# Kernel optimization log

Hardware: AMD Instinct MI355X
Metric: run time of the kernel (lower is better)

Reference implementation:

```python
import jax, jax.numpy as jnp
import numpy as np

D_MODEL = 256      # num_nodes == d_model (forced by pre_relation mask shape)
MW = 2             # moving_window (hardcoded '2' in MPNN reshape)
STRIDE = 1
DECAY = 0.7
INPUT_DIM = 64
OUTPUT_DIM = 64
BN_EPS = 1e-5


def _mask_matrix():
    # Mask_Matrix: block (i,j) of size d_model x d_model equals decay**|i-j|
    blocks = DECAY ** np.abs(np.arange(MW)[:, None] - np.arange(MW)[None, :])
    return jnp.asarray(np.kron(blocks, np.ones((D_MODEL, D_MODEL))).astype(np.float32))


def _bn(h, w, b):
    # training-mode BatchNorm1d over channel-last layout [B, N, C]
    mu = h.mean(axis=(0, 1))
    var = h.var(axis=(0, 1))  # biased variance, as torch uses for normalization
    return (h - mu) * jax.lax.rsqrt(var + BN_EPS) * w + b


def setup_inputs() -> dict:
    key = jax.random.key(0)
    ks = jax.random.split(key, 4)
    bs, scale_num = 16, 17
    x = jax.random.normal(ks[0], (bs, scale_num, D_MODEL, INPUT_DIM), jnp.float32)
    # mapping2 weights scaled small to keep the dot-product softmax well conditioned
    w_map2 = jax.random.normal(ks[1], (INPUT_DIM, INPUT_DIM), jnp.float32) * 0.05
    b_map2 = jnp.zeros((INPUT_DIM,), jnp.float32)
    bn0_w = jnp.ones((INPUT_DIM,), jnp.float32)
    bn0_b = jnp.zeros((INPUT_DIM,), jnp.float32)
    th0_w = jax.random.normal(ks[2], (OUTPUT_DIM, INPUT_DIM), jnp.float32) / np.float32(np.sqrt(INPUT_DIM))
    th0_b = jnp.zeros((OUTPUT_DIM,), jnp.float32)
    th1_w = jax.random.normal(ks[3], (OUTPUT_DIM, INPUT_DIM), jnp.float32) / np.float32(np.sqrt(INPUT_DIM))
    th1_b = jnp.zeros((OUTPUT_DIM,), jnp.float32)
    bn1_w = jnp.ones((OUTPUT_DIM,), jnp.float32)
    bn1_b = jnp.zeros((OUTPUT_DIM,), jnp.float32)
    return dict(x=x, w_map2=w_map2, b_map2=b_map2, bn0_w=bn0_w, bn0_b=bn0_b,
                th0_w=th0_w, th0_b=th0_b, th1_w=th1_w, th1_b=th1_b,
                bn1_w=bn1_w, bn1_b=bn1_b)


def reference(x, w_map2, b_map2, bn0_w, bn0_b, th0_w, th0_b, th1_w, th1_b, bn1_w, bn1_b):
    bs, S, N, F = x.shape
    L = (S - MW) // STRIDE + 1  # num_windows from F.unfold
    # WindowConv_Graph + transpose(2,3) + reshape: X[b,l,m,n,f] = x[b, l*stride+m, n, f]
    idx = np.arange(L)[:, None] * STRIDE + np.arange(MW)[None, :]
    X = x[:, idx].reshape(bs * L, MW * N, F)  # [B', N1, F]

    # Dot_Graph_Construction_weights (N1 != d_model -> mapping2 branch)
    nf = X @ w_map2.T + b_map2                       # [B', N1, F]
    adj = jnp.einsum('bnf,bmf->bnm', nf, nf)         # [B', N1, N1]
    eye = jnp.eye(MW * N, dtype=x.dtype)
    adj = jax.nn.leaky_relu(adj - eye * 1e8)
    adj = jax.nn.softmax(adj, axis=-1) + eye

    # decay mask multiply
    adj = adj * _mask_matrix()

    # BatchNorm over input_dim channels
    xb = _bn(nf, bn0_w, bn0_b)

    # MPNN_mk_v2, field=2, way='sum'
    out = (adj @ xb) @ th0_w.T + th0_b               # hop 1
    adj2 = adj @ adj
    out = out + (adj2 @ xb) @ th1_w.T + th1_b        # hop 2
    out = jax.nn.leaky_relu(_bn(out, bn1_w, bn1_b))

    # pooling over the moving_window axis (mean), then over windows (mean)
    out = out.reshape(bs, L, MW, N, OUTPUT_DIM).mean(axis=2)
    return out.mean(axis=1)  # [bs, num_nodes, output_dim]
```

## Files before the change

kernel.cpp:

```cpp
#include <hip/hip_runtime.h>


typedef unsigned short u16;
typedef __bf16 bf16x8 __attribute__((ext_vector_type(8)));
typedef float f32x4 __attribute__((ext_vector_type(4)));
typedef unsigned int u32x4 __attribute__((ext_vector_type(4)));

#define MFMA16(a, b, c) __builtin_amdgcn_mfma_f32_16x16x32_bf16(a, b, c, 0, 0, 0)

#define BSZ 16
#define SNUM 17
#define FD 64
#define NB 256
#define N1 512
#define SL_ELEMS 16384
#define Y_ELEMS (BSZ * SNUM * SL_ELEMS)

#define WM_O 0
#define BM_O 4096
#define B0W_O 4160
#define B0B_O 4224
#define T0W_O 4288
#define T0B_O 8384
#define T1W_O 8448
#define T1B_O 12544
#define B1W_O 12608
#define B1B_O 12672
#define P_TOT 12736

#define SLAB2_O 32768
#define RED_O 65536
#define SCR_O 65792
#define LDS_U16 (SCR_O + 16 * 640)

__device__ __forceinline__ float bf2f(u16 u) {
    union { unsigned int i; float f; } v;
    v.i = ((unsigned int)u) << 16;
    return v.f;
}
__device__ __forceinline__ u16 f2bu(float f) {
    __bf16 h = (__bf16)f;
    return __builtin_bit_cast(u16, h);
}
__device__ __forceinline__ u16 f2bf(float f) {
    unsigned int u = __builtin_bit_cast(unsigned int, f);
    unsigned int r = (u + 0x7fffu + ((u >> 16) & 1u)) >> 16;
    return (u16)r;
}
__device__ __forceinline__ bf16x8 ld8g(const u16* p) {
    return __builtin_bit_cast(bf16x8, *reinterpret_cast<const u32x4*>(p));
}

__global__ __launch_bounds__(256) void k_prep(
    const void* p0, const void* p1, const void* p2, const void* p3,
    const void* p4, const void* p5, const void* p6, const void* p7,
    const void* p8, const void* p9, int* __restrict__ flagOut,
    u16* __restrict__ pc, float* __restrict__ stats) {
    const int tid = threadIdx.x, lane = tid & 63;
    int z = 0, bc = 0;
    const unsigned int* w = (const unsigned int*)p0;
    for (int i = lane; i < 2048; i += 64) {
        const unsigned int v = w[i];
        z += ((v & 0xffffu) == 0u);
        bc += (v >> 14) & 1;
    }
#pragma unroll
    for (int o = 1; o < 64; o <<= 1) {
        z += __shfl_xor(z, o);
        bc += __shfl_xor(bc, o);
    }
    const int flag = (z > 1024 || bc > 256) ? 1 : 0;
    if (blockIdx.x == 0) {
        if (tid == 0) *flagOut = flag;
        if (tid < 256) stats[tid] = 0.f;
    }
    const int i = blockIdx.x * 256 + tid;
    if (i >= P_TOT) return;
    const void* src;
    int si;
    if (i < BM_O)        { src = p0; si = i; }
    else if (i < B0W_O)  { src = p1; si = i - BM_O; }
    else if (i < B0B_O)  { src = p2; si = i - B0W_O; }
    else if (i < T0W_O)  { src = p3; si = i - B0B_O; }
    else if (i < T0B_O)  { src = p4; si = i - T0W_O; }
    else if (i < T1W_O)  { src = p5; si = i - T0B_O; }
    else if (i < T1B_O)  { src = p6; si = i - T1W_O; }
    else if (i < B1W_O)  { src = p7; si = i - T1B_O; }
    else if (i < B1B_O)  { src = p8; si = i - B1W_O; }
    else                 { src = p9; si = i - B1B_O; }
    pc[i] = flag ? f2bf(((const float*)src)[si]) : ((const u16*)src)[si];
}

__global__ __launch_bounds__(256) void k_y(const void* __restrict__ xv,
                                           const int* __restrict__ flag,
                                           const u16* __restrict__ pc,
                                           u16* __restrict__ y,
                                           float* __restrict__ gstats) {
    const int slice = blockIdx.x;
    const int tid = threadIdx.x, wave = tid >> 6, lane = tid & 63;
    const int quad = lane >> 4, l16 = lane & 15;
    __shared__ float red[128];
    if (tid < 128) red[tid] = 0.f;
    const int isf32 = *flag;

    f32x4 acc[4][4];
#pragma unroll
    for (int i = 0; i < 4; i++)
#pragma unroll
        for (int j = 0; j < 4; j++) acc[i][j] = (f32x4){0.f, 0.f, 0.f, 0.f};

    bf16x8 bfr[4][2];
#pragma unroll
    for (int nt = 0; nt < 4; nt++)
#pragma unroll
        for (int kh = 0; kh < 2; kh++)
            bfr[nt][kh] = ld8g(pc + WM_O + (nt * 16 + l16) * 64 + kh * 32 + quad * 8);

    const float* xf = (const float*)xv + (size_t)slice * SL_ELEMS;
    const u16* xh = (const u16*)xv + (size_t)slice * SL_ELEMS;

#pragma unroll
    for (int mt = 0; mt < 4; mt++) {
        const int row = wave * 64 + mt * 16 + l16;
        bf16x8 a0, a1;
        if (isf32) {
            const float* r0 = xf + row * 64 + quad * 8;
            f32x4 v0 = *(const f32x4*)r0;
            f32x4 v1 = *(const f32x4*)(r0 + 4);
            f32x4 v2 = *(const f32x4*)(r0 + 32);
            f32x4 v3 = *(const f32x4*)(r0 + 36);
#pragma unroll
            for (int j = 0; j < 4; j++) {
                a0[j] = (__bf16)v0[j]; a0[4 + j] = (__bf16)v1[j];
                a1[j] = (__bf16)v2[j]; a1[4 + j] = (__bf16)v3[j];
            }
        } else {
            a0 = ld8g(xh + row * 64 + quad * 8);
            a1 = ld8g(xh + row * 64 + 32 + quad * 8);
        }
#pragma unroll
        for (int nt = 0; nt < 4; nt++)
            acc[mt][nt] = MFMA16(a1, bfr[nt][1], MFMA16(a0, bfr[nt][0], acc[mt][nt]));
    }

    u16* ys = y + (size_t)slice * SL_ELEMS;
    float s1[4] = {0.f, 0.f, 0.f, 0.f}, s2[4] = {0.f, 0.f, 0.f, 0.f};
#pragma unroll
    for (int nt = 0; nt < 4; nt++) {
        const int col = nt * 16 + l16;
        const float bias = bf2f(pc[BM_O + col]);
#pragma unroll
        for (int mt = 0; mt < 4; mt++)
#pragma unroll
            for (int r = 0; r < 4; r++) {
                const int row = wave * 64 + mt * 16 + quad * 4 + r;
                const float v = acc[mt][nt][r] + bias;
                ys[row * 64 + col] = f2bu(v);
                s1[nt] += v;
                s2[nt] += v * v;
            }
        s1[nt] += __shfl_xor(s1[nt], 16); s1[nt] += __shfl_xor(s1[nt], 32);
        s2[nt] += __shfl_xor(s2[nt], 16); s2[nt] += __shfl_xor(s2[nt], 32);
    }
    __syncthreads();
    if (quad == 0) {
#pragma unroll
        for (int nt = 0; nt < 4; nt++) {
            atomicAdd(&red[nt * 16 + l16], s1[nt]);
            atomicAdd(&red[64 + nt * 16 + l16], s2[nt]);
        }
    }
    __syncthreads();
    const int s = slice % SNUM;
    const float wgt = (s == 0 || s == SNUM - 1) ? 1.f : 2.f;
    if (tid < 128) atomicAdd(&gstats[tid], red[tid] * wgt);
}

__global__ __launch_bounds__(1024)
__attribute__((amdgpu_waves_per_eu(4, 4)))
void k_mega(
    const u16* __restrict__ y, float* __restrict__ stats,
    const u16* __restrict__ pc, u16* __restrict__ opre) {
    __shared__ u16 lds[LDS_U16];
    u16* slab1 = lds;
    u16* slab2 = lds + SLAB2_O;
    float* red = (float*)(lds + RED_O);
    const int tid = threadIdx.x, w = tid >> 6, lane = tid & 63;
    const int quad = lane >> 4, l16 = lane & 15;
    u16* scr = lds + SCR_O + w * 640;
    const int p = blockIdx.x, b = p >> 4, l = p & 15;
    const f32x4 ZERO4 = (f32x4){0.f, 0.f, 0.f, 0.f};

    if (tid < 128) red[tid] = 0.f;

    const float cinv = 1.f / 131072.f;
    const int fme = tid & 63;
    float mu0 = stats[fme] * cinv;
    float vr0 = fmaxf(stats[64 + fme] * cinv - mu0 * mu0, 0.f);
    const float scale_f = rsqrtf(vr0 + 1e-5f) * bf2f(pc[B0W_O + fme]);
    const float shift_f = bf2f(pc[B0B_O + fme]) - mu0 * scale_f;

    const u16* ybase = y + (size_t)(b * SNUM + l) * SL_ELEMS;
#pragma unroll
    for (int i = 0; i < 4; i++) {
        const int gid = i * 1024 + tid, n = gid >> 3, g = gid & 7;
        *(u32x4*)(slab1 + n * 64 + ((g ^ (n & 7)) << 3)) =
            *(const u32x4*)(ybase + n * 64 + g * 8);
    }
    __syncthreads();

#pragma unroll
    for (int i = 0; i < 4; i++) {
        const int gn = (tid >> 6) + i * 16;
        union { u16 u[8]; u32x4 v; } pk;
#pragma unroll
        for (int j = 0; j < 8; j++) {
            const int n = gn * 8 + j;
            const u16 raw = slab1[n * 64 + (((fme >> 3) ^ (n & 7)) << 3) + (fme & 7)];
            pk.u[j] = f2bu(bf2f(raw) * scale_f + shift_f);
        }
        *(u32x4*)(slab2 + fme * 512 + ((gn ^ fme) << 3)) = pk.v;
    }
    __syncthreads();

    bf16x8 a[2][2];
#pragma unroll
    for (int st = 0; st < 2; st++)
#pragma unroll
        for (int h = 0; h < 2; h++) {
            const int row = w * 32 + st * 16 + l16;
            a[st][h] = *(const bf16x8*)(slab1 + row * 64 + (((h * 4 + quad) ^ (row & 7)) << 3));
        }

    const float mb = (w < 8) ? 0.7f : (1.0f / 0.7f);
    const float me = (w < 8) ? (1.0f / 0.7f) : 1.0f;

#pragma unroll 1
    for (int pass = 0; pass < 2; pass++) {
        f32x4 oacc[2][4];
        f32x4 lsum[2];
#pragma unroll
        for (int st = 0; st < 2; st++) {
            lsum[st] = ZERO4;
#pragma unroll
            for (int ft = 0; ft < 4; ft++) oacc[st][ft] = ZERO4;
        }

#pragma unroll 1
        for (int c = 0; c < 8; c++) {
            if (c == 4) {
#pragma unroll
                for (int st = 0; st < 2; st++)
#pragma unroll
                    for (int r = 0; r < 4; r++) lsum[st][r] *= mb;
            }
            const float lmf = ((w >= 8) == (c >= 4)) ? 0.f : -0.5145731728f;
#pragma unroll
            for (int ch = 0; ch < 2; ch++) {
                const int colbase = c * 64 + ch * 32;
                f32x4 S[2][2];
#pragma unroll
                for (int jt = 0; jt < 2; jt++) {
                    const int rj = colbase + jt * 16 + l16;
                    const bf16x8 b0 = *(const bf16x8*)(slab1 + rj * 64 + ((quad ^ (rj & 7)) << 3));
                    const bf16x8 b1 = *(const bf16x8*)(slab1 + rj * 64 + (((4 + quad) ^ (rj & 7)) << 3));
#pragma unroll
                    for (int st = 0; st < 2; st++)
                        S[st][jt] = MFMA16(a[st][1], b1, MFMA16(a[st][0], b0, ZERO4));
                }
                bf16x8 pa[2];
#pragma unroll
                for (int st = 0; st < 2; st++) {
                    const int rowbase = w * 32 + st * 16;
#pragma unroll
                    for (int jt = 0; jt < 2; jt++)
#pragma unroll
                        for (int r = 0; r < 4; r++) {
                            const float s = S[st][jt][r];
                            const float m2 = s > 0.f ? 1.44269504f : 0.0144269504f;
                            float pv = exp2f(fminf(fmaf(s, m2, lmf), 86.f));
                            if (colbase + jt * 16 == rowbase && l16 == quad * 4 + r) pv = 0.f;
                            lsum[st][r] += pv;
                            scr[(quad * 4 + r) * 40 + jt * 16 + l16] = f2bu(pv);
                        }
                    pa[st] = *(const bf16x8*)(scr + l16 * 40 + quad * 8);
                }
#pragma unroll
                for (int ft = 0; ft < 4; ft++) {
                    const int f = ft * 16 + l16, gn = c * 8 + ch * 4 + quad;
                    const bf16x8 bv = *(const bf16x8*)(slab2 + f * 512 + ((gn ^ f) << 3));
                    oacc[0][ft] = MFMA16(pa[0], bv, oacc[0][ft]);
                    oacc[1][ft] = MFMA16(pa[1], bv, oacc[1][ft]);
                }
            }
        }
#pragma unroll
        for (int st = 0; st < 2; st++)
#pragma unroll
            for (int r = 0; r < 4; r++) {
                lsum[st][r] += __shfl_xor(lsum[st][r], 1);
                lsum[st][r] += __shfl_xor(lsum[st][r], 2);
                lsum[st][r] += __shfl_xor(lsum[st][r], 4);
                lsum[st][r] += __shfl_xor(lsum[st][r], 8);
            }

        if (pass == 0) {
#pragma unroll
            for (int st = 0; st < 2; st++) {
                f32x4 inv;
#pragma unroll
                for (int r = 0; r < 4; r++) inv[r] = __builtin_amdgcn_rcpf(lsum[st][r] * me);
#pragma unroll
                for (int ft = 0; ft < 4; ft++)
#pragma unroll
                    for (int r = 0; r < 4; r++) {
                        const int i = w * 32 + st * 16 + quad * 4 + r;
                        const int f = ft * 16 + l16;
                        const float xbv = bf2f(slab2[f * 512 + (((i >> 3) ^ f) << 3) + (i & 7)]);
                        oacc[st][ft][r] = oacc[st][ft][r] * inv[r] + xbv;
                    }
            }
            __syncthreads();
#pragma unroll
            for (int st = 0; st < 2; st++)
#pragma unroll
                for (int ft = 0; ft < 4; ft++)
#pragma unroll
                    for (int r = 0; r < 4; r++) {
                        const int i = w * 32 + st * 16 + quad * 4 + r;
                        const int f = ft * 16 + l16;
                        slab2[f * 512 + (((i >> 3) ^ f) << 3) + (i & 7)] = f2bu(oacc[st][ft][r]);
                    }
            __syncthreads();
        } else {
            float s1a[4] = {0.f, 0.f, 0.f, 0.f}, s2a[4] = {0.f, 0.f, 0.f, 0.f};
#pragma unroll
            for (int st = 0; st < 2; st++) {
                f32x4 inv;
#pragma unroll
                for (int r = 0; r < 4; r++) inv[r] = __builtin_amdgcn_rcpf(lsum[st][r] * me);
#pragma unroll
                for (int ft = 0; ft < 4; ft++)
#pragma unroll
                    for (int r = 0; r < 4; r++) {
                        const int i = w * 32 + st * 16 + quad * 4 + r;
                        const int f = ft * 16 + l16;
                        const float o1 = bf2f(slab2[f * 512 + (((i >> 3) ^ f) << 3) + (i & 7)]);
                        oacc[st][ft][r] = oacc[st][ft][r] * inv[r] + o1;
                    }
                bf16x8 a1[2], a2[2];
                const int irow = w * 32 + st * 16 + l16;
#pragma unroll
                for (int h = 0; h < 2; h++)
#pragma unroll
                    for (int j = 0; j < 8; j++) {
                        const int f = h * 32 + quad * 8 + j;
                        const u16 raw = slab2[f * 512 + (((irow >> 3) ^ f) << 3) + (irow & 7)];
                        a1[h][j] = __builtin_bit_cast(__bf16, raw);
                    }
#pragma unroll
                for (int h = 0; h < 2; h++) {
#pragma unroll
                    for (int ftl = 0; ftl < 2; ftl++)
#pragma unroll
                        for (int r = 0; r < 4; r++)
                            scr[(quad * 4 + r) * 40 + ftl * 16 + l16] = f2bu(oacc[st][2 * h + ftl][r]);
                    a2[h] = *(const bf16x8*)(scr + l16 * 40 + quad * 8);
                }
                f32x4 pacc[4];
#pragma unroll
                for (int ot = 0; ot < 4; ot++) {
                    const int o = ot * 16 + l16;
                    const float bias = bf2f(pc[T0B_O + o]) + bf2f(pc[T1B_O + o]);
                    pacc[ot] = (f32x4){bias, bias, bias, bias};
                }
#pragma unroll
                for (int h = 0; h < 2; h++)
#pragma unroll
                    for (int ot = 0; ot < 4; ot++) {
                        const int o = ot * 16 + l16;
                        bf16x8 w0f = ld8g(pc + T0W_O + o * 64 + h * 32 + quad * 8);
                        bf16x8 w1f = ld8g(pc + T1W_O + o * 64 + h * 32 + quad * 8);
                        pacc[ot] = MFMA16(a1[h], w0f, pacc[ot]);
                        pacc[ot] = MFMA16(a2[h], w1f, pacc[ot]);
                    }
#pragma unroll
                for (int ot = 0; ot < 4; ot++)
#pragma unroll
                    for (int r = 0; r < 4; r++) {
                        const int i = w * 32 + st * 16 + quad * 4 + r;
                        const int o = ot * 16 + l16;
                        const float v = pacc[ot][r];
                        s1a[ot] += v;
                        s2a[ot] += v * v;
                        opre[(size_t)p * (N1 * FD) + (size_t)i * 64 + o] = f2bu(v);
                    }
            }
#pragma unroll
            for (int ot = 0; ot < 4; ot++) {
                s1a[ot] += __shfl_xor(s1a[ot], 16); s1a[ot] += __shfl_xor(s1a[ot], 32);
                s2a[ot] += __shfl_xor(s2a[ot], 16); s2a[ot] += __shfl_xor(s2a[ot], 32);
            }
            if (quad == 0) {
#pragma unroll
                for (int ot = 0; ot < 4; ot++) {
                    atomicAdd(&red[ot * 16 + l16], s1a[ot]);
                    atomicAdd(&red[64 + ot * 16 + l16], s2a[ot]);
                }
            }
            __syncthreads();
            if (tid < 128) atomicAdd(&stats[128 + tid], red[tid]);
        }
    }
}

__global__ __launch_bounds__(256) void k_final(const u16* __restrict__ op,
                                               const float* __restrict__ stats,
                                               const u16* __restrict__ pc,
                                               float* __restrict__ out) {
    const int o = blockIdx.x * 256 + threadIdx.x;
    const int f = o & 63, n = (o >> 6) & 255, b = o >> 14;
    const float inv = 1.f / 131072.f;
    const float mu = stats[128 + f] * inv;
    const float var = fmaxf(stats[192 + f] * inv - mu * mu, 0.f);
    const float rs = rsqrtf(var + 1e-5f);
    const float scale = rs * bf2f(pc[B1W_O + f]);
    const float shift = bf2f(pc[B1B_O + f]) - mu * scale;
    float acc = 0.f;
    for (int l = 0; l < 16; l++) {
        const size_t pb = (size_t)(b * 16 + l) * N1 * FD;
#pragma unroll
        for (int m = 0; m < 2; m++) {
            float v = bf2f(op[pb + (size_t)(m * 256 + n) * 64 + f]);
            v = v * scale + shift;
            acc += (v > 0.f ? v : 0.01f * v);
        }
    }
    out[o] = acc * (1.f / 32.f);
}

extern "C" void kernel_launch(void* const* d_in, const int* in_sizes, int n_in,
                              void* d_out, int out_size, void* d_ws, size_t ws_size,
                              hipStream_t stream) {
    char* ws = (char*)d_ws;
    size_t off = 0;
    auto alloc = [&](size_t bytes) { void* pp = ws + off; off += (bytes + 255) & ~(size_t)255; return pp; };
    u16* y = (u16*)alloc((size_t)Y_ELEMS * 2);
    u16* opre = (u16*)alloc((size_t)NB * N1 * FD * 2);
    u16* pc = (u16*)alloc(P_TOT * 2);
    float* stats = (float*)alloc(256 * 4);
    int* flag = (int*)alloc(256);
    float* out = (float*)d_out;

    k_prep<<<50, 256, 0, stream>>>(d_in[1], d_in[2], d_in[3], d_in[4], d_in[5],
                                   d_in[6], d_in[7], d_in[8], d_in[9], d_in[10],
                                   flag, pc, stats);
    k_y<<<BSZ * SNUM, 256, 0, stream>>>(d_in[0], flag, pc, y, stats);
    k_mega<<<NB, 1024, 0, stream>>>(y, stats, pc, opre);
    k_final<<<1024, 256, 0, stream>>>(opre, stats, pc, out);
}
```

Baseline: 200.8 us.

## Split mega kernel into two hop kernels with row-half blocks

Replaces the single k_mega kernel (256 blocks, each handling all 512 rows over two hop passes) with two kernels launched over 512 blocks, where each block handles one 256-row half. The first hop result is written to a global z1 image and reloaded by the second kernel, which also recomputes the staging of the input slab. The aim is to fill more CUs, since 256 blocks of 1024 threads underuse the device. In exchange it adds an extra launch, a global round trip for the intermediate, and duplicated score and softmax computation across the two kernels.

```diff
diff --git a/kernel.cpp b/kernel.cpp
--- a/kernel.cpp
+++ b/kernel.cpp
@@ -176,11 +176,154 @@
     if (tid < 128) atomicAdd(&gstats[tid], red[tid] * wgt);
 }
 
+__device__ __forceinline__ void stage_slab1(u16* slab1, const u16* ybase,
+                                            int tid) {
+#pragma unroll
+    for (int i = 0; i < 4; i++) {
+        const int gid = i * 1024 + tid, n = gid >> 3, g = gid & 7;
+        *(u32x4*)(slab1 + n * 64 + ((g ^ (n & 7)) << 3)) =
+            *(const u32x4*)(ybase + n * 64 + g * 8);
+    }
+}
+
 __global__ __launch_bounds__(1024)
 __attribute__((amdgpu_waves_per_eu(4, 4)))
-void k_mega(
-    const u16* __restrict__ y, float* __restrict__ stats,
-    const u16* __restrict__ pc, u16* __restrict__ opre) {
+void k_h1(const u16* __restrict__ y, const float* __restrict__ stats,
+          const u16* __restrict__ pc, u16* __restrict__ z1img) {
+    __shared__ u16 lds[LDS_U16];
+    u16* slab1 = lds;
+    u16* slab2 = lds + SLAB2_O;
+    const int tid = threadIdx.x, w = tid >> 6, lane = tid & 63;
+    const int quad = lane >> 4, l16 = lane & 15;
+    u16* scr = lds + SCR_O + w * 640;
+    const int g = blockIdx.x, p = g >> 1, half = g & 1;
+    const int b = p >> 4, l = p & 15;
+    const f32x4 ZERO4 = (f32x4){0.f, 0.f, 0.f, 0.f};
+
+    const float cinv = 1.f / 131072.f;
+    const int fme = tid & 63;
+    float mu0 = stats[fme] * cinv;
+    float vr0 = fmaxf(stats[64 + fme] * cinv - mu0 * mu0, 0.f);
+    const float scale_f = rsqrtf(vr0 + 1e-5f) * bf2f(pc[B0W_O + fme]);
+    const float shift_f = bf2f(pc[B0B_O + fme]) - mu0 * scale_f;
+
+    const u16* ybase = y + (size_t)(b * SNUM + l) * SL_ELEMS;
+    stage_slab1(slab1, ybase, tid);
+    __syncthreads();
+
+#pragma unroll
+    for (int i = 0; i < 4; i++) {
+        const int gn = (tid >> 6) + i * 16;
+        union { u16 u[8]; u32x4 v; } pk;
+#pragma unroll
+        for (int j = 0; j < 8; j++) {
+            const int n = gn * 8 + j;
+            const u16 raw = slab1[n * 64 + (((fme >> 3) ^ (n & 7)) << 3) + (fme & 7)];
+            pk.u[j] = f2bu(bf2f(raw) * scale_f + shift_f);
+        }
+        *(u32x4*)(slab2 + fme * 512 + ((gn ^ fme) << 3)) = pk.v;
+    }
+    __syncthreads();
+
+    const int rowbase = half * 256 + w * 16;
+    bf16x8 a[2];
+#pragma unroll
+    for (int h = 0; h < 2; h++) {
+        const int row = rowbase + l16;
+        a[h] = *(const bf16x8*)(slab1 + row * 64 + (((h * 4 + quad) ^ (row & 7)) << 3));
+    }
+
+    const float mb = (half == 0) ? 0.7f : (1.0f / 0.7f);
+    const float me = (half == 0) ? (1.0f / 0.7f) : 1.0f;
+
+    f32x4 oacc[4];
+    f32x4 lsum = ZERO4;
+#pragma unroll
+    for (int ft = 0; ft < 4; ft++) oacc[ft] = ZERO4;
+
+#pragma unroll 1
+    for (int c = 0; c < 8; c++) {
+        if (c == 4) {
+#pragma unroll
+            for (int r = 0; r < 4; r++) lsum[r] *= mb;
+        }
+        const float lmf = ((half == 1) == (c >= 4)) ? 0.f : -0.5145731728f;
+#pragma unroll
+        for (int ch = 0; ch < 2; ch++) {
+            const int colbase = c * 64 + ch * 32;
+            f32x4 S[2];
+#pragma unroll
+            for (int jt = 0; jt < 2; jt++) {
+                const int rj = colbase + jt * 16 + l16;
+                const bf16x8 b0 = *(const bf16x8*)(slab1 + rj * 64 + ((quad ^ (rj & 7)) << 3));
+                const bf16x8 b1 = *(const bf16x8*)(slab1 + rj * 64 + (((4 + quad) ^ (rj & 7)) << 3));
+                S[jt] = MFMA16(a[1], b1, MFMA16(a[0], b0, ZERO4));
+            }
+#pragma unroll
+            for (int jt = 0; jt < 2; jt++)
+#pragma unroll
+                for (int r = 0; r < 4; r++) {
+                    const float s = S[jt][r];
+                    const float m2 = s > 0.f ? 1.44269504f : 0.0144269504f;
+                    float pv = exp2f(fminf(fmaf(s, m2, lmf), 86.f));
+                    if (colbase + jt * 16 == rowbase && l16 == quad * 4 + r) pv = 0.f;
+                    lsum[r] += pv;
+                    scr[(quad * 4 + r) * 40 + jt * 16 + l16] = f2bu(pv);
+                }
+            const bf16x8 pa = *(const bf16x8*)(scr + l16 * 40 + quad * 8);
+#pragma unroll
+            for (int ft = 0; ft < 4; ft++) {
+                const int f = ft * 16 + l16, gn = c * 8 + ch * 4 + quad;
+                const bf16x8 bv = *(const bf16x8*)(slab2 + f * 512 + ((gn ^ f) << 3));
+                oacc[ft] = MFMA16(pa, bv, oacc[ft]);
+            }
+        }
+    }
+#pragma unroll
+    for (int r = 0; r < 4; r++) {
+        lsum[r] += __shfl_xor(lsum[r], 1);
+        lsum[r] += __shfl_xor(lsum[r], 2);
+        lsum[r] += __shfl_xor(lsum[r], 4);
+        lsum[r] += __shfl_xor(lsum[r], 8);
+    }
+
+    f32x4 inv;
+#pragma unroll
+    for (int r = 0; r < 4; r++) inv[r] = __builtin_amdgcn_rcpf(lsum[r] * me);
+#pragma unroll
+    for (int ft = 0; ft < 4; ft++)
+#pragma unroll
+        for (int r = 0; r < 4; r++) {
+            const int i = rowbase + quad * 4 + r;
+            const int f = ft * 16 + l16;
+            const float xbv = bf2f(slab2[f * 512 + (((i >> 3) ^ f) << 3) + (i & 7)]);
+            oacc[ft][r] = oacc[ft][r] * inv[r] + xbv;
+        }
+    __syncthreads();
+#pragma unroll
+    for (int ft = 0; ft < 4; ft++)
+#pragma unroll
+        for (int r = 0; r < 4; r++) {
+            const int i = rowbase + quad * 4 + r;
+            const int f = ft * 16 + l16;
+            slab2[f * 512 + (((i >> 3) ^ f) << 3) + (i & 7)] = f2bu(oacc[ft][r]);
+        }
+    __syncthreads();
+    {
+        const int fr = tid >> 4, seg = tid & 15;
+        const int off = (((half * 32) ^ (fr & 32)) << 3) + seg * 16;
+        u16* dst = z1img + (size_t)p * 32768 + fr * 512 + off;
+        const u16* srcp = slab2 + fr * 512 + off;
+        *(u32x4*)(dst) = *(const u32x4*)(srcp);
+        *(u32x4*)(dst + 8) = *(const u32x4*)(srcp + 8);
+    }
+}
+
+__global__ __launch_bounds__(1024)
+__attribute__((amdgpu_waves_per_eu(4, 4)))
+void k_h2(const u16* __restrict__ y, const u16* __restrict__ z1img,
+          float* __restrict__ stats, const u16* __restrict__ pc,
+          u16* __restrict__ opre) {
     __shared__ u16 lds[LDS_U16];
     u16* slab1 = lds;
     u16* slab2 = lds + SLAB2_O;
@@ -188,230 +331,159 @@
     const int tid = threadIdx.x, w = tid >> 6, lane = tid & 63;
     const int quad = lane >> 4, l16 = lane & 15;
     u16* scr = lds + SCR_O + w * 640;
-    const int p = blockIdx.x, b = p >> 4, l = p & 15;
+    const int g = blockIdx.x, p = g >> 1, half = g & 1;
+    const int b = p >> 4, l = p & 15;
     const f32x4 ZERO4 = (f32x4){0.f, 0.f, 0.f, 0.f};
 
     if (tid < 128) red[tid] = 0.f;
 
-    const float cinv = 1.f / 131072.f;
-    const int fme = tid & 63;
-    float mu0 = stats[fme] * cinv;
-    float vr0 = fmaxf(stats[64 + fme] * cinv - mu0 * mu0, 0.f);
-    const float scale_f = rsqrtf(vr0 + 1e-5f) * bf2f(pc[B0W_O + fme]);
-    const float shift_f = bf2f(pc[B0B_O + fme]) - mu0 * scale_f;
-
     const u16* ybase = y + (size_t)(b * SNUM + l) * SL_ELEMS;
+    stage_slab1(slab1, ybase, tid);
+
+    const u16* zsrc = z1img + (size_t)p * 32768;
 #pragma unroll
     for (int i = 0; i < 4; i++) {
-        const int gid = i * 1024 + tid, n = gid >> 3, g = gid & 7;
-        *(u32x4*)(slab1 + n * 64 + ((g ^ (n & 7)) << 3)) =
-            *(const u32x4*)(ybase + n * 64 + g * 8);
-    }
-    __syncthreads();
-
-#pragma unroll
-    for (int i = 0; i < 4; i++) {
-        const int gn = (tid >> 6) + i * 16;
-        union { u16 u[8]; u32x4 v; } pk;
+        const int gid = i * 1024 + tid;
+        *(u32x4*)(slab2 + gid * 8) = *(const u32x4*)(zsrc + gid * 8);
+    }
+    __syncthreads();
+
+    const int rowbase = half * 256 + w * 16;
+    bf16x8 a[2];
+#pragma unroll
+    for (int h = 0; h < 2; h++) {
+        const int row = rowbase + l16;
+        a[h] = *(const bf16x8*)(slab1 + row * 64 + (((h * 4 + quad) ^ (row & 7)) << 3));
+    }
+
+    const float mb = (half == 0) ? 0.7f : (1.0f / 0.7f);
+    const float me = (half == 0) ? (1.0f / 0.7f) : 1.0f;
+
+    f32x4 oacc[4];
+    f32x4 lsum = ZERO4;
+#pragma unroll
+    for (int ft = 0; ft < 4; ft++) oacc[ft] = ZERO4;
+
+#pragma unroll 1
+    for (int c = 0; c < 8; c++) {
+        if (c == 4) {
+#pragma unroll
+            for (int r = 0; r < 4; r++) lsum[r] *= mb;
+        }
+        const float lmf = ((half == 1) == (c >= 4)) ? 0.f : -0.5145731728f;
+#pragma unroll
+        for (int ch = 0; ch < 2; ch++) {
+            const int colbase = c * 64 + ch * 32;
+            f32x4 S[2];
+#pragma unroll
+            for (int jt = 0; jt < 2; jt++) {
+                const int rj = colbase + jt * 16 + l16;
+                const bf16x8 b0 = *(const bf16x8*)(slab1 + rj * 64 + ((quad ^ (rj & 7)) << 3));
+                const bf16x8 b1 = *(const bf16x8*)(slab1 + rj * 64 + (((4 + quad) ^ (rj & 7)) << 3));
+                S[jt] = MFMA16(a[1], b1, MFMA16(a[0], b0, ZERO4));
+            }
+#pragma unroll
+            for (int jt = 0; jt < 2; jt++)
+#pragma unroll
+                for (int r = 0; r < 4; r++) {
+                    const float s = S[jt][r];
+                    const float m2 = s > 0.f ? 1.44269504f : 0.0144269504f;
+                    float pv = exp2f(fminf(fmaf(s, m2, lmf), 86.f));
+                    if (colbase + jt * 16 == rowbase && l16 == quad * 4 + r) pv = 0.f;
+                    lsum[r] += pv;
+                    scr[(quad * 4 + r) * 40 + jt * 16 + l16] = f2bu(pv);
+                }
+            const bf16x8 pa = *(const bf16x8*)(scr + l16 * 40 + quad * 8);
+#pragma unroll
+            for (int ft = 0; ft < 4; ft++) {
+                const int f = ft * 16 + l16, gn = c * 8 + ch * 4 + quad;
+                const bf16x8 bv = *(const bf16x8*)(slab2 + f * 512 + ((gn ^ f) << 3));
+                oacc[ft] = MFMA16(pa, bv, oacc[ft]);
+            }
+        }
+    }
+#pragma unroll
+    for (int r = 0; r < 4; r++) {
+        lsum[r] += __shfl_xor(lsum[r], 1);
+        lsum[r] += __shfl_xor(lsum[r], 2);
+        lsum[r] += __shfl_xor(lsum[r], 4);
+        lsum[r] += __shfl_xor(lsum[r], 8);
+    }
+
+    float s1a[4] = {0.f, 0.f, 0.f, 0.f}, s2a[4] = {0.f, 0.f, 0.f, 0.f};
+    f32x4 inv;
+#pragma unroll
+    for (int r = 0; r < 4; r++) inv[r] = __builtin_amdgcn_rcpf(lsum[r] * me);
+#pragma unroll
+    for (int ft = 0; ft < 4; ft++)
+#pragma unroll
+        for (int r = 0; r < 4; r++) {
+            const int i = rowbase + quad * 4 + r;
+            const int f = ft * 16 + l16;
+            const float o1 = bf2f(slab2[f * 512 + (((i >> 3) ^ f) << 3) + (i & 7)]);
+            oacc[ft][r] = oacc[ft][r] * inv[r] + o1;
+        }
+    bf16x8 a1[2], a2[2];
+    const int irow = rowbase + l16;
+#pragma unroll
+    for (int h = 0; h < 2; h++)
 #pragma unroll
         for (int j = 0; j < 8; j++) {
-            const int n = gn * 8 + j;
-            const u16 raw = slab1[n * 64 + (((fme >> 3) ^ (n & 7)) << 3) + (fme & 7)];
-            pk.u[j] = f2bu(bf2f(raw) * scale_f + shift_f);
-        }
-        *(u32x4*)(slab2 + fme * 512 + ((gn ^ fme) << 3)) = pk.v;
-    }
-    __syncthreads();
-
-    bf16x8 a[2][2];
-#pragma unroll
-    for (int st = 0; st < 2; st++)
-#pragma unroll
-        for (int h = 0; h < 2; h++) {
-            const int row = w * 32 + st * 16 + l16;
-            a[st][h] = *(const bf16x8*)(slab1 + row * 64 + (((h * 4 + quad) ^ (row & 7)) << 3));
-        }
-
-    const float mb = (w < 8) ? 0.7f : (1.0f / 0.7f);
-    const float me = (w < 8) ? (1.0f / 0.7f) : 1.0f;
-
-#pragma unroll 1
-    for (int pass = 0; pass < 2; pass++) {
-        f32x4 oacc[2][4];
-        f32x4 lsum[2];
-#pragma unroll
-        for (int st = 0; st < 2; st++) {
-            lsum[st] = ZERO4;
-#pragma unroll
-            for (int ft = 0; ft < 4; ft++) oacc[st][ft] = ZERO4;
-        }
-
-#pragma unroll 1
-        for (int c = 0; c < 8; c++) {
-            if (c == 4) {
-#pragma unroll
-                for (int st = 0; st < 2; st++)
-#pragma unroll
-                    for (int r = 0; r < 4; r++) lsum[st][r] *= mb;
-            }
-            const float lmf = ((w >= 8) == (c >= 4)) ? 0.f : -0.5145731728f;
-#pragma unroll
-            for (int ch = 0; ch < 2; ch++) {
-                const int colbase = c * 64 + ch * 32;
-                f32x4 S[2][2];
-#pragma unroll
-                for (int jt = 0; jt < 2; jt++) {
-                    const int rj = colbase + jt * 16 + l16;
-                    const bf16x8 b0 = *(const bf16x8*)(slab1 + rj * 64 + ((quad ^ (rj & 7)) << 3));
-                    const bf16x8 b1 = *(const bf16x8*)(slab1 + rj * 64 + (((4 + quad) ^ (rj & 7)) << 3));
-#pragma unroll
-                    for (int st = 0; st < 2; st++)
-                        S[st][jt] = MFMA16(a[st][1], b1, MFMA16(a[st][0], b0, ZERO4));
-                }
-                bf16x8 pa[2];
-#pragma unroll
-                for (int st = 0; st < 2; st++) {
-                    const int rowbase = w * 32 + st * 16;
-#pragma unroll
-                    for (int jt = 0; jt < 2; jt++)
-#pragma unroll
-                        for (int r = 0; r < 4; r++) {
-                            const float s = S[st][jt][r];
-                            const float m2 = s > 0.f ? 1.44269504f : 0.0144269504f;
-                            float pv = exp2f(fminf(fmaf(s, m2, lmf), 86.f));
-                            if (colbase + jt * 16 == rowbase && l16 == quad * 4 + r) pv = 0.f;
-                            lsum[st][r] += pv;
-                            scr[(quad * 4 + r) * 40 + jt * 16 + l16] = f2bu(pv);
-                        }
-                    pa[st] = *(const bf16x8*)(scr + l16 * 40 + quad * 8);
-                }
-#pragma unroll
-                for (int ft = 0; ft < 4; ft++) {
-                    const int f = ft * 16 + l16, gn = c * 8 + ch * 4 + quad;
-                    const bf16x8 bv = *(const bf16x8*)(slab2 + f * 512 + ((gn ^ f) << 3));
-                    oacc[0][ft] = MFMA16(pa[0], bv, oacc[0][ft]);
-                    oacc[1][ft] = MFMA16(pa[1], bv, oacc[1][ft]);
-                }
-            }
-        }
-#pragma unroll
-        for (int st = 0; st < 2; st++)
-#pragma unroll
-            for (int r = 0; r < 4; r++) {
-                lsum[st][r] += __shfl_xor(lsum[st][r], 1);
-                lsum[st][r] += __shfl_xor(lsum[st][r], 2);
-                lsum[st][r] += __shfl_xor(lsum[st][r], 4);
-                lsum[st][r] += __shfl_xor(lsum[st][r], 8);
-            }
-
-        if (pass == 0) {
-#pragma unroll
-            for (int st = 0; st < 2; st++) {
-                f32x4 inv;
-#pragma unroll
-                for (int r = 0; r < 4; r++) inv[r] = __builtin_amdgcn_rcpf(lsum[st][r] * me);
-#pragma unroll
-                for (int ft = 0; ft < 4; ft++)
-#pragma unroll
-                    for (int r = 0; r < 4; r++) {
-                        const int i = w * 32 + st * 16 + quad * 4 + r;
-                        const int f = ft * 16 + l16;
-                        const float xbv = bf2f(slab2[f * 512 + (((i >> 3) ^ f) << 3) + (i & 7)]);
-                        oacc[st][ft][r] = oacc[st][ft][r] * inv[r] + xbv;
-                    }
-            }
-            __syncthreads();
-#pragma unroll
-            for (int st = 0; st < 2; st++)
-#pragma unroll
-                for (int ft = 0; ft < 4; ft++)
-#pragma unroll
-                    for (int r = 0; r < 4; r++) {
-                        const int i = w * 32 + st * 16 + quad * 4 + r;
-                        const int f = ft * 16 + l16;
-                        slab2[f * 512 + (((i >> 3) ^ f) << 3) + (i & 7)] = f2bu(oacc[st][ft][r]);
-                    }
-            __syncthreads();
-        } else {
-            float s1a[4] = {0.f, 0.f, 0.f, 0.f}, s2a[4] = {0.f, 0.f, 0.f, 0.f};
-#pragma unroll
-            for (int st = 0; st < 2; st++) {
-                f32x4 inv;
-#pragma unroll
-                for (int r = 0; r < 4; r++) inv[r] = __builtin_amdgcn_rcpf(lsum[st][r] * me);
-#pragma unroll
-                for (int ft = 0; ft < 4; ft++)
-#pragma unroll
-                    for (int r = 0; r < 4; r++) {
-                        const int i = w * 32 + st * 16 + quad * 4 + r;
-                        const int f = ft * 16 + l16;
-                        const float o1 = bf2f(slab2[f * 512 + (((i >> 3) ^ f) << 3) + (i & 7)]);
-                        oacc[st][ft][r] = oacc[st][ft][r] * inv[r] + o1;
-                    }
-                bf16x8 a1[2], a2[2];
-                const int irow = w * 32 + st * 16 + l16;
-#pragma unroll
-                for (int h = 0; h < 2; h++)
-#pragma unroll
-                    for (int j = 0; j < 8; j++) {
-                        const int f = h * 32 + quad * 8 + j;
-                        const u16 raw = slab2[f * 512 + (((irow >> 3) ^ f) << 3) + (irow & 7)];
-                        a1[h][j] = __builtin_bit_cast(__bf16, raw);
-                    }
-#pragma unroll
-                for (int h = 0; h < 2; h++) {
-#pragma unroll
-                    for (int ftl = 0; ftl < 2; ftl++)
-#pragma unroll
-                        for (int r = 0; r < 4; r++)
-                            scr[(quad * 4 + r) * 40 + ftl * 16 + l16] = f2bu(oacc[st][2 * h + ftl][r]);
-                    a2[h] = *(const bf16x8*)(scr + l16 * 40 + quad * 8);
-                }
-                f32x4 pacc[4];
-#pragma unroll
-                for (int ot = 0; ot < 4; ot++) {
-                    const int o = ot * 16 + l16;
-                    const float bias = bf2f(pc[T0B_O + o]) + bf2f(pc[T1B_O + o]);
-                    pacc[ot] = (f32x4){bias, bias, bias, bias};
-                }
-#pragma unroll
-                for (int h = 0; h < 2; h++)
-#pragma unroll
-                    for (int ot = 0; ot < 4; ot++) {
-                        const int o = ot * 16 + l16;
-                        bf16x8 w0f = ld8g(pc + T0W_O + o * 64 + h * 32 + quad * 8);
-                        bf16x8 w1f = ld8g(pc + T1W_O + o * 64 + h * 32 + quad * 8);
-                        pacc[ot] = MFMA16(a1[h], w0f, pacc[ot]);
-                        pacc[ot] = MFMA16(a2[h], w1f, pacc[ot]);
-                    }
-#pragma unroll
-                for (int ot = 0; ot < 4; ot++)
-#pragma unroll
-                    for (int r = 0; r < 4; r++) {
-                        const int i = w * 32 + st * 16 + quad * 4 + r;
-                        const int o = ot * 16 + l16;
-                        const float v = pacc[ot][r];
-                        s1a[ot] += v;
-                        s2a[ot] += v * v;
-                        opre[(size_t)p * (N1 * FD) + (size_t)i * 64 + o] = f2bu(v);
-                    }
-            }
-#pragma unroll
-            for (int ot = 0; ot < 4; ot++) {
-                s1a[ot] += __shfl_xor(s1a[ot], 16); s1a[ot] += __shfl_xor(s1a[ot], 32);
-                s2a[ot] += __shfl_xor(s2a[ot], 16); s2a[ot] += __shfl_xor(s2a[ot], 32);
-            }
-            if (quad == 0) {
-#pragma unroll
-                for (int ot = 0; ot < 4; ot++) {
-                    atomicAdd(&red[ot * 16 + l16], s1a[ot]);
-                    atomicAdd(&red[64 + ot * 16 + l16], s2a[ot]);
-                }
-            }
-            __syncthreads();
-            if (tid < 128) atomicAdd(&stats[128 + tid], red[tid]);
-        }
-    }
+            const int f = h * 32 + quad * 8 + j;
+            const u16 raw = slab2[f * 512 + (((irow >> 3) ^ f) << 3) + (irow & 7)];
+            a1[h][j] = __builtin_bit_cast(__bf16, raw);
+        }
+#pragma unroll
+    for (int h = 0; h < 2; h++) {
+#pragma unroll
+        for (int ftl = 0; ftl < 2; ftl++)
+#pragma unroll
+            for (int r = 0; r < 4; r++)
+                scr[(quad * 4 + r) * 40 + ftl * 16 + l16] = f2bu(oacc[2 * h + ftl][r]);
+        a2[h] = *(const bf16x8*)(scr + l16 * 40 + quad * 8);
+    }
+    f32x4 pacc[4];
+#pragma unroll
+    for (int ot = 0; ot < 4; ot++) {
+        const int o = ot * 16 + l16;
+        const float bias = bf2f(pc[T0B_O + o]) + bf2f(pc[T1B_O + o]);
+        pacc[ot] = (f32x4){bias, bias, bias, bias};
+    }
+#pragma unroll
+    for (int h = 0; h < 2; h++)
+#pragma unroll
+        for (int ot = 0; ot < 4; ot++) {
+            const int o = ot * 16 + l16;
+            bf16x8 w0f = ld8g(pc + T0W_O + o * 64 + h * 32 + quad * 8);
+            bf16x8 w1f = ld8g(pc + T1W_O + o * 64 + h * 32 + quad * 8);
+            pacc[ot] = MFMA16(a1[h], w0f, pacc[ot]);
+            pacc[ot] = MFMA16(a2[h], w1f, pacc[ot]);
+        }
+#pragma unroll
+    for (int ot = 0; ot < 4; ot++)
+#pragma unroll
+        for (int r = 0; r < 4; r++) {
+            const int i = rowbase + quad * 4 + r;
+            const int o = ot * 16 + l16;
+            const float v = pacc[ot][r];
+            s1a[ot] += v;
+            s2a[ot] += v * v;
+            opre[(size_t)p * (N1 * FD) + (size_t)i * 64 + o] = f2bu(v);
+        }
+#pragma unroll
+    for (int ot = 0; ot < 4; ot++) {
+        s1a[ot] += __shfl_xor(s1a[ot], 16); s1a[ot] += __shfl_xor(s1a[ot], 32);
+        s2a[ot] += __shfl_xor(s2a[ot], 16); s2a[ot] += __shfl_xor(s2a[ot], 32);
+    }
+    if (quad == 0) {
+#pragma unroll
+        for (int ot = 0; ot < 4; ot++) {
+            atomicAdd(&red[ot * 16 + l16], s1a[ot]);
+            atomicAdd(&red[64 + ot * 16 + l16], s2a[ot]);
+        }
+    }
+    __syncthreads();
+    if (tid < 128) atomicAdd(&stats[128 + tid], red[tid]);
 }
 
 __global__ __launch_bounds__(256) void k_final(const u16* __restrict__ op,
@@ -446,6 +518,7 @@
     size_t off = 0;
     auto alloc = [&](size_t bytes) { void* pp = ws + off; off += (bytes + 255) & ~(size_t)255; return pp; };
     u16* y = (u16*)alloc((size_t)Y_ELEMS * 2);
+    u16* z1img = (u16*)alloc((size_t)NB * 32768 * 2);
     u16* opre = (u16*)alloc((size_t)NB * N1 * FD * 2);
     u16* pc = (u16*)alloc(P_TOT * 2);
     float* stats = (float*)alloc(256 * 4);
@@ -456,6 +529,7 @@
                                    d_in[6], d_in[7], d_in[8], d_in[9], d_in[10],
                                    flag, pc, stats);
     k_y<<<BSZ * SNUM, 256, 0, stream>>>(d_in[0], flag, pc, y, stats);
-    k_mega<<<NB, 1024, 0, stream>>>(y, stats, pc, opre);
+    k_h1<<<2 * NB, 1024, 0, stream>>>(y, stats, pc, z1img);
+    k_h2<<<2 * NB, 1024, 0, stream>>>(y, z1img, stats, pc, opre);
     k_final<<<1024, 256, 0, stream>>>(opre, stats, pc, out);
 }
```

After: 210.2 us. +4.7%, slower.
